# Kernel optimization log

Hardware: AMD Instinct MI355X
Metric: run time of the kernel (lower is better)

The kernel has to match this reference:

```python
import jax, jax.numpy as jnp
import numpy as np
from functools import partial

SUBJECT_CATEGORY_ID = 0
PNMS_THRESH = 0.7


def box_cxcywh_to_xyxy(b):
    cx, cy, w, h = jnp.split(b, 4, axis=-1)
    return jnp.concatenate([cx - 0.5 * w, cy - 0.5 * h, cx + 0.5 * w, cy + 0.5 * h], axis=-1)


def box_iou(b1, b2):
    # b1: [Q,4], b2: [Q,4] (xyxy) -> [Q,Q] IoU (torchvision-style)
    area1 = (b1[:, 2] - b1[:, 0]) * (b1[:, 3] - b1[:, 1])
    area2 = (b2[:, 2] - b2[:, 0]) * (b2[:, 3] - b2[:, 1])
    lt = jnp.maximum(b1[:, None, :2], b2[None, :, :2])
    rb = jnp.minimum(b1[:, None, 2:], b2[None, :, 2:])
    wh = jnp.clip(rb - lt, 0.0)
    inter = wh[..., 0] * wh[..., 1]
    union = area1[:, None] + area2[None, :] - inter
    return inter / union


def pnms_one(vs, ol, pair_iou):
    # vs: [Q,V] verb scores, ol: [Q] int labels, pair_iou: [Q,Q].
    # Replicates the original greedy per-class suppression, including the
    # original's row-i update vs[i, suppressed_queries] -= 1 (requires Q <= V).
    Q, V = vs.shape

    def class_step(vs, i):
        col = jnp.take(vs, i, axis=1)           # [Q]
        order = jnp.argsort(-col)               # descending, like reversed argsort

        def greedy(carry, j):
            alive, supp = carry
            is_alive = alive[j]
            kill = alive & (ol == ol[j]) & (pair_iou[j] > PNMS_THRESH)
            kill = kill.at[j].set(False)
            kill = kill & is_alive
            alive_next = (alive & ~kill).at[j].set(False)
            alive = jnp.where(is_alive, alive_next, alive)
            return (alive, supp | kill), None

        (alive, supp), _ = jax.lax.scan(
            greedy, (jnp.ones((Q,), bool), jnp.zeros((Q,), bool)), order)
        delta = jnp.zeros((V,), vs.dtype).at[:Q].set(supp.astype(vs.dtype))
        vs = vs.at[i].add(-delta)
        return vs, None

    vs, _ = jax.lax.scan(class_step, vs, jnp.arange(V))
    return vs


def setup_inputs() -> dict:
    key = jax.random.key(0)
    k1, k2, k3, k4, k5 = jax.random.split(key, 5)
    B, Q, C, V = 1024, 100, 81, 117
    return {
        'obj_logits': jax.random.normal(k1, (B, Q, C), jnp.float32),
        'verb_logits': jax.random.normal(k2, (B, Q, V), jnp.float32),
        'sub_boxes': jax.random.uniform(k3, (B, Q, 4), jnp.float32),
        'obj_boxes': jax.random.uniform(k4, (B, Q, 4), jnp.float32),
        'target_sizes': jax.random.randint(k5, (B, 2), 0, 1333, jnp.int32),
    }


def reference(obj_logits, verb_logits, sub_boxes, obj_boxes, target_sizes):
    obj_prob = jax.nn.softmax(obj_logits, axis=-1)
    obj_scores = obj_prob[..., :-1].max(-1)                 # [B,Q]
    obj_labels = jnp.argmax(obj_prob[..., :-1], axis=-1)    # [B,Q]
    verb_scores = jax.nn.sigmoid(verb_logits)               # [B,Q,V]

    sizes = target_sizes.astype(jnp.float32)
    img_h, img_w = sizes[:, 0], sizes[:, 1]
    scale = jnp.stack([img_w, img_h, img_w, img_h], axis=1)  # [B,4]
    sb = box_cxcywh_to_xyxy(sub_boxes) * scale[:, None, :]
    ob = box_cxcywh_to_xyxy(obj_boxes) * scale[:, None, :]

    sub_labels = jnp.full_like(obj_labels, SUBJECT_CATEGORY_ID)
    labels = jnp.concatenate([sub_labels, obj_labels], axis=1)   # [B,2Q]
    boxes = jnp.concatenate([sb, ob], axis=1)                    # [B,2Q,4]

    vs = verb_scores * obj_scores[..., None]                     # [B,Q,V]
    pair_iou = jnp.minimum(jax.vmap(box_iou)(sb, sb), jax.vmap(box_iou)(ob, ob))
    vs = jax.vmap(pnms_one)(vs, obj_labels, pair_iou)
    return vs, obj_scores, labels, boxes
```

## Files before the change

kernel.cpp:

```cpp
#include <hip/hip_runtime.h>
#include <math.h>

#define Q 100
#define NC 81
#define NV 117
#define MAXK 48

__global__ __launch_bounds__(256) void k_scores_vs(
    const float*  __restrict__ obj_logits,
    const float4* __restrict__ verb4,
    float* __restrict__ out_vs,
    float* __restrict__ out_scores,
    float* __restrict__ out_labels,
    int BQ)
{
    const int lane = threadIdx.x & 63;
    const int sl   = lane & 15;
    const int w    = blockIdx.x * 4 + (threadIdx.x >> 6);
    const int q    = w * 4 + (lane >> 4);
    if (q >= BQ) return;
    const float* lp = obj_logits + (size_t)q * NC;

    float v[5];
    #pragma unroll
    for (int c = 0; c < 5; ++c) v[c] = lp[sl + c * 16];
    const float l80 = lp[80];

    float bv = v[0]; int bi = sl;
    #pragma unroll
    for (int c = 1; c < 5; ++c)
        if (v[c] > bv) { bv = v[c]; bi = sl + c * 16; }
    #pragma unroll
    for (int d = 1; d < 16; d <<= 1) {
        float ov = __shfl_xor(bv, d, 16);
        int   oi = __shfl_xor(bi, d, 16);
        if (ov > bv || (ov == bv && oi < bi)) { bv = ov; bi = oi; }
    }
    const float m = fmaxf(bv, l80);

    float s = (sl == 0) ? expf(l80 - m) : 0.f;
    #pragma unroll
    for (int c = 0; c < 5; ++c) s += expf(v[c] - m);
    #pragma unroll
    for (int d = 1; d < 16; d <<= 1) s += __shfl_xor(s, d, 16);

    const float sc = __fdiv_rn(expf(bv - m), s);
    if (sl == 0) {
        int b = q / Q, qq = q - b * Q;
        out_scores[q] = sc;
        out_labels[(size_t)b * 2 * Q + qq]     = 0.0f;
        out_labels[(size_t)b * 2 * Q + Q + qq] = (float)bi;
    }

    const float s0 = __shfl(sc, 0);
    const float s1 = __shfl(sc, 16);
    const float s2 = __shfl(sc, 32);
    const float s3 = __shfl(sc, 48);

    const size_t base4 = (size_t)w * NV;
    float4* ovs4 = reinterpret_cast<float4*>(out_vs);
    #pragma unroll
    for (int it = 0; it < 2; ++it) {
        const int idx = it * 64 + lane;
        if (idx < NV) {
            float4 x = verb4[base4 + idx];
            float xv[4] = {x.x, x.y, x.z, x.w};
            float r[4];
            #pragma unroll
            for (int j = 0; j < 4; ++j) {
                const int e = idx * 4 + j;
                const float scq = (e < NV) ? s0 : (e < 2 * NV) ? s1
                                 : (e < 3 * NV) ? s2 : s3;
                float sg = __fdiv_rn(1.0f, __fadd_rn(1.0f, expf(-xv[j])));
                r[j] = __fmul_rn(sg, scq);
            }
            ovs4[base4 + idx] = make_float4(r[0], r[1], r[2], r[3]);
        }
    }
}

__global__ __launch_bounds__(256) void k_pnms(
    const float* __restrict__ sub_boxes,
    const float* __restrict__ obj_boxes,
    const int*   __restrict__ target_sizes,
    const float* __restrict__ out_labels,
    float* __restrict__ out_vs,
    float* __restrict__ out_boxes)
{
    __shared__ float4 sb4[Q], ob4[Q];
    __shared__ float  area_s[Q], area_o[Q];
    __shared__ int    labi[Q];
    __shared__ unsigned long long lbl_bits[NC - 1][2];
    __shared__ unsigned long long mask_s[2 * Q];
    __shared__ unsigned long long killset_s[2 * Q];
    __shared__ int   clist_s[Q];
    __shared__ float col_s[Q];
    __shared__ float vsrow[MAXK * 101];
    __shared__ int   anyconf, Ksh;

    const int b   = blockIdx.x;
    const int tid = threadIdx.x;

    if (tid == 0) anyconf = 0;
    if (tid < 2 * Q) killset_s[tid] = 0ull;
    if (tid < 2 * (NC - 1)) ((unsigned long long*)lbl_bits)[tid] = 0ull;

    if (tid < 2 * Q) {
        const int q = (tid < Q) ? tid : tid - Q;
        const float fh = (float)target_sizes[2 * b];
        const float fw = (float)target_sizes[2 * b + 1];
        const float4* src = reinterpret_cast<const float4*>(tid < Q ? sub_boxes : obj_boxes);
        float4 cxy = src[(size_t)b * Q + q];
        float hw = __fmul_rn(0.5f, cxy.z);
        float hh = __fmul_rn(0.5f, cxy.w);
        float4 box;
        box.x = __fmul_rn(__fsub_rn(cxy.x, hw), fw);
        box.y = __fmul_rn(__fsub_rn(cxy.y, hh), fh);
        box.z = __fmul_rn(__fadd_rn(cxy.x, hw), fw);
        box.w = __fmul_rn(__fadd_rn(cxy.y, hh), fh);
        float area = __fmul_rn(__fsub_rn(box.z, box.x), __fsub_rn(box.w, box.y));
        if (tid < Q) {
            sb4[q] = box; area_s[q] = area;
            reinterpret_cast<float4*>(out_boxes)[(size_t)b * 2 * Q + q] = box;
            labi[q] = (int)out_labels[(size_t)b * 2 * Q + Q + q];
        } else {
            ob4[q] = box; area_o[q] = area;
            reinterpret_cast<float4*>(out_boxes)[(size_t)b * 2 * Q + Q + q] = box;
        }
    }
    __syncthreads();

    if (tid < Q)
        atomicOr(&lbl_bits[labi[tid]][tid >> 6], 1ull << (tid & 63));
    __syncthreads();

    if (tid < Q) {
        const int j = tid;
        const float4 sj = sb4[j]; const float asj = area_s[j];
        const float4 oj = ob4[j]; const float aoj = area_o[j];
        const int lj = labi[j];
        unsigned long long bits[2] = {0ull, 0ull};
        #pragma unroll
        for (int w = 0; w < 2; ++w) {
            unsigned long long mm = lbl_bits[lj][w];
            if (w == (j >> 6)) mm &= ~(1ull << (j & 63));
            while (mm) {
                int kb = __builtin_ctzll(mm); mm &= mm - 1;
                int k = kb + w * 64;
                float4 sk = sb4[k];
                float wx = fmaxf(__fsub_rn(fminf(sj.z, sk.z), fmaxf(sj.x, sk.x)), 0.f);
                float wy = fmaxf(__fsub_rn(fminf(sj.w, sk.w), fmaxf(sj.y, sk.y)), 0.f);
                float inter = __fmul_rn(wx, wy);
                float uni = __fsub_rn(__fadd_rn(asj, area_s[k]), inter);
                float ious = __fdiv_rn(inter, uni);
                float4 ok = ob4[k];
                wx = fmaxf(__fsub_rn(fminf(oj.z, ok.z), fmaxf(oj.x, ok.x)), 0.f);
                wy = fmaxf(__fsub_rn(fminf(oj.w, ok.w), fmaxf(oj.y, ok.y)), 0.f);
                inter = __fmul_rn(wx, wy);
                uni = __fsub_rn(__fadd_rn(aoj, area_o[k]), inter);
                float iouo = __fdiv_rn(inter, uni);
                if (ious != ious || iouo != iouo) continue;
                if (fminf(ious, iouo) > 0.7f) bits[w] |= 1ull << kb;
            }
        }
        mask_s[2 * j]     = bits[0];
        mask_s[2 * j + 1] = bits[1];
        if (bits[0] | bits[1]) anyconf = 1;
    }
    __syncthreads();

    if (!anyconf) return;

    if (tid == 0) {
        int K = 0;
        for (int q = 0; q < Q; ++q)
            if (mask_s[2 * q] | mask_s[2 * q + 1]) clist_s[K++] = q;
        Ksh = K;
    }
    __syncthreads();
    const int K = Ksh;
    const bool staged = (K <= MAXK);

    if (staged) {
        for (int idx = tid; idx < K * Q; idx += 256) {
            int k = idx / Q, i = idx - k * Q;
            vsrow[k * 101 + i] = out_vs[(size_t)b * Q * NV + clist_s[k] * NV + i];
        }
    }
    __syncthreads();

    if (tid == 0) {
        for (int i = 0; i < Q; ++i) {
            for (int k = 0; k < K; ++k) {
                int c = clist_s[k];
                float v = staged ? vsrow[k * 101 + i]
                                 : out_vs[(size_t)b * Q * NV + c * NV + i];
                if ((killset_s[2 * c + (i >> 6)] >> (i & 63)) & 1ull)
                    v = __fsub_rn(v, 1.0f);
                col_s[k] = v;
            }
            unsigned long long alive0 = ~0ull, alive1 = (1ull << 36) - 1;
            unsigned long long supp0 = 0ull, supp1 = 0ull;
            for (int t = 0; t < K; ++t) {
                float best = col_s[0]; int bk = 0;
                for (int k = 1; k < K; ++k) { float ck = col_s[k]; if (ck > best) { best = ck; bk = k; } }
                col_s[bk] = -3.0e38f;
                int q = clist_s[bk];
                bool al = (q < 64) ? ((alive0 >> q) & 1ull) : ((alive1 >> (q - 64)) & 1ull);
                if (al) {
                    unsigned long long m0 = mask_s[2 * q], m1 = mask_s[2 * q + 1];
                    supp0 |= alive0 & m0;
                    supp1 |= alive1 & m1;
                    alive0 &= ~m0;
                    alive1 &= ~m1;
                    if (q < 64) alive0 &= ~(1ull << q); else alive1 &= ~(1ull << (q - 64));
                }
            }
            killset_s[2 * i]     = supp0;
            killset_s[2 * i + 1] = supp1;
        }
    }
    __syncthreads();

    for (int idx = tid; idx < Q * Q; idx += 256) {
        int qrow = idx / Q, v = idx - qrow * Q;
        if ((killset_s[2 * qrow + (v >> 6)] >> (v & 63)) & 1ull) {
            size_t a = (size_t)b * Q * NV + qrow * NV + v;
            out_vs[a] = __fsub_rn(out_vs[a], 1.0f);
        }
    }
}

extern "C" void kernel_launch(void* const* d_in, const int* in_sizes, int n_in,
                              void* d_out, int out_size, void* d_ws, size_t ws_size,
                              hipStream_t stream) {
    const float* obj_logits   = (const float*)d_in[0];
    const float* verb_logits  = (const float*)d_in[1];
    const float* sub_boxes    = (const float*)d_in[2];
    const float* obj_boxes    = (const float*)d_in[3];
    const int*   target_sizes = (const int*)d_in[4];
    const int B  = in_sizes[0] / (Q * NC);
    const int BQ = B * Q;

    float* out_vs     = (float*)d_out;
    float* out_scores = out_vs + (size_t)B * Q * NV;
    float* out_labels = out_scores + (size_t)BQ;
    float* out_boxes  = out_labels + (size_t)B * 2 * Q;

    k_scores_vs<<<dim3((BQ + 15) / 16), dim3(256), 0, stream>>>(
        obj_logits, (const float4*)verb_logits,
        out_vs, out_scores, out_labels, BQ);

    k_pnms<<<dim3(B), dim3(256), 0, stream>>>(
        sub_boxes, obj_boxes, target_sizes, out_labels, out_vs, out_boxes);
}
```

Measured before the change: 133.4 us.

## Fuse score/verb kernel into per-image PNMS kernel with 512 threads

```diff
diff --git a/kernel.cpp b/kernel.cpp
--- a/kernel.cpp
+++ b/kernel.cpp
@@ -5,91 +5,23 @@
 #define NC 81
 #define NV 117
 #define MAXK 48
-
-__global__ __launch_bounds__(256) void k_scores_vs(
+#define NV4 2925
+
+__global__ __launch_bounds__(512) void hoi_fused(
     const float*  __restrict__ obj_logits,
     const float4* __restrict__ verb4,
+    const float*  __restrict__ sub_boxes,
+    const float*  __restrict__ obj_boxes,
+    const int*    __restrict__ target_sizes,
     float* __restrict__ out_vs,
     float* __restrict__ out_scores,
     float* __restrict__ out_labels,
-    int BQ)
-{
-    const int lane = threadIdx.x & 63;
-    const int sl   = lane & 15;
-    const int w    = blockIdx.x * 4 + (threadIdx.x >> 6);
-    const int q    = w * 4 + (lane >> 4);
-    if (q >= BQ) return;
-    const float* lp = obj_logits + (size_t)q * NC;
-
-    float v[5];
-    #pragma unroll
-    for (int c = 0; c < 5; ++c) v[c] = lp[sl + c * 16];
-    const float l80 = lp[80];
-
-    float bv = v[0]; int bi = sl;
-    #pragma unroll
-    for (int c = 1; c < 5; ++c)
-        if (v[c] > bv) { bv = v[c]; bi = sl + c * 16; }
-    #pragma unroll
-    for (int d = 1; d < 16; d <<= 1) {
-        float ov = __shfl_xor(bv, d, 16);
-        int   oi = __shfl_xor(bi, d, 16);
-        if (ov > bv || (ov == bv && oi < bi)) { bv = ov; bi = oi; }
-    }
-    const float m = fmaxf(bv, l80);
-
-    float s = (sl == 0) ? expf(l80 - m) : 0.f;
-    #pragma unroll
-    for (int c = 0; c < 5; ++c) s += expf(v[c] - m);
-    #pragma unroll
-    for (int d = 1; d < 16; d <<= 1) s += __shfl_xor(s, d, 16);
-
-    const float sc = __fdiv_rn(expf(bv - m), s);
-    if (sl == 0) {
-        int b = q / Q, qq = q - b * Q;
-        out_scores[q] = sc;
-        out_labels[(size_t)b * 2 * Q + qq]     = 0.0f;
-        out_labels[(size_t)b * 2 * Q + Q + qq] = (float)bi;
-    }
-
-    const float s0 = __shfl(sc, 0);
-    const float s1 = __shfl(sc, 16);
-    const float s2 = __shfl(sc, 32);
-    const float s3 = __shfl(sc, 48);
-
-    const size_t base4 = (size_t)w * NV;
-    float4* ovs4 = reinterpret_cast<float4*>(out_vs);
-    #pragma unroll
-    for (int it = 0; it < 2; ++it) {
-        const int idx = it * 64 + lane;
-        if (idx < NV) {
-            float4 x = verb4[base4 + idx];
-            float xv[4] = {x.x, x.y, x.z, x.w};
-            float r[4];
-            #pragma unroll
-            for (int j = 0; j < 4; ++j) {
-                const int e = idx * 4 + j;
-                const float scq = (e < NV) ? s0 : (e < 2 * NV) ? s1
-                                 : (e < 3 * NV) ? s2 : s3;
-                float sg = __fdiv_rn(1.0f, __fadd_rn(1.0f, expf(-xv[j])));
-                r[j] = __fmul_rn(sg, scq);
-            }
-            ovs4[base4 + idx] = make_float4(r[0], r[1], r[2], r[3]);
-        }
-    }
-}
-
-__global__ __launch_bounds__(256) void k_pnms(
-    const float* __restrict__ sub_boxes,
-    const float* __restrict__ obj_boxes,
-    const int*   __restrict__ target_sizes,
-    const float* __restrict__ out_labels,
-    float* __restrict__ out_vs,
     float* __restrict__ out_boxes)
 {
+    __shared__ float  score_s[Q];
+    __shared__ int    labi[Q];
     __shared__ float4 sb4[Q], ob4[Q];
     __shared__ float  area_s[Q], area_o[Q];
-    __shared__ int    labi[Q];
     __shared__ unsigned long long lbl_bits[NC - 1][2];
     __shared__ unsigned long long mask_s[2 * Q];
     __shared__ unsigned long long killset_s[2 * Q];
@@ -98,12 +30,47 @@
     __shared__ float vsrow[MAXK * 101];
     __shared__ int   anyconf, Ksh;
 
-    const int b   = blockIdx.x;
-    const int tid = threadIdx.x;
+    const int b    = blockIdx.x;
+    const int tid  = threadIdx.x;
+    const int lane = tid & 63;
+    const int sl   = lane & 15;
+    const int r16  = tid >> 4;
 
     if (tid == 0) anyconf = 0;
     if (tid < 2 * Q) killset_s[tid] = 0ull;
     if (tid < 2 * (NC - 1)) ((unsigned long long*)lbl_bits)[tid] = 0ull;
+
+    for (int qi = r16; qi < Q; qi += 32) {
+        const float* lp = obj_logits + ((size_t)b * Q + qi) * NC;
+        float v[5];
+        #pragma unroll
+        for (int c = 0; c < 5; ++c) v[c] = lp[sl + c * 16];
+        const float l80 = lp[80];
+
+        float bv = v[0]; int bi = sl;
+        #pragma unroll
+        for (int c = 1; c < 5; ++c)
+            if (v[c] > bv) { bv = v[c]; bi = sl + c * 16; }
+        #pragma unroll
+        for (int d = 1; d < 16; d <<= 1) {
+            float ov = __shfl_xor(bv, d, 16);
+            int   oi = __shfl_xor(bi, d, 16);
+            if (ov > bv || (ov == bv && oi < bi)) { bv = ov; bi = oi; }
+        }
+        const float m = fmaxf(bv, l80);
+
+        float s = (sl == 0) ? __expf(l80 - m) : 0.f;
+        #pragma unroll
+        for (int c = 0; c < 5; ++c) s += __expf(v[c] - m);
+        #pragma unroll
+        for (int d = 1; d < 16; d <<= 1) s += __shfl_xor(s, d, 16);
+
+        if (sl == 0) {
+            score_s[qi] = __fmul_rn(__expf(bv - m), __builtin_amdgcn_rcpf(s));
+            labi[qi] = bi;
+        }
+    }
+    __syncthreads();
 
     if (tid < 2 * Q) {
         const int q = (tid < Q) ? tid : tid - Q;
@@ -119,19 +86,32 @@
         box.z = __fmul_rn(__fadd_rn(cxy.x, hw), fw);
         box.w = __fmul_rn(__fadd_rn(cxy.y, hh), fh);
         float area = __fmul_rn(__fsub_rn(box.z, box.x), __fsub_rn(box.w, box.y));
-        if (tid < Q) {
-            sb4[q] = box; area_s[q] = area;
-            reinterpret_cast<float4*>(out_boxes)[(size_t)b * 2 * Q + q] = box;
-            labi[q] = (int)out_labels[(size_t)b * 2 * Q + Q + q];
-        } else {
-            ob4[q] = box; area_o[q] = area;
-            reinterpret_cast<float4*>(out_boxes)[(size_t)b * 2 * Q + Q + q] = box;
-        }
-    }
-    __syncthreads();
-
-    if (tid < Q)
+        if (tid < Q) { sb4[q] = box; area_s[q] = area; }
+        else         { ob4[q] = box; area_o[q] = area; }
+        reinterpret_cast<float4*>(out_boxes)[(size_t)b * 2 * Q + tid] = box;
+        out_labels[(size_t)b * 2 * Q + tid] = (tid < Q) ? 0.0f : (float)labi[q];
+    }
+    if (tid < Q) {
+        out_scores[(size_t)b * Q + tid] = score_s[tid];
         atomicOr(&lbl_bits[labi[tid]][tid >> 6], 1ull << (tid & 63));
+    }
+
+    {
+        const size_t base4 = (size_t)b * NV4;
+        float4* ovs4 = reinterpret_cast<float4*>(out_vs);
+        for (int idx = tid; idx < NV4; idx += 512) {
+            float4 x = verb4[base4 + idx];
+            float xv[4] = {x.x, x.y, x.z, x.w};
+            float r[4];
+            #pragma unroll
+            for (int j = 0; j < 4; ++j) {
+                int lq = (idx * 4 + j) / NV;
+                float sg = __builtin_amdgcn_rcpf(__fadd_rn(1.0f, __expf(-xv[j])));
+                r[j] = __fmul_rn(sg, score_s[lq]);
+            }
+            ovs4[base4 + idx] = make_float4(r[0], r[1], r[2], r[3]);
+        }
+    }
     __syncthreads();
 
     if (tid < Q) {
@@ -182,7 +162,7 @@
     const bool staged = (K <= MAXK);
 
     if (staged) {
-        for (int idx = tid; idx < K * Q; idx += 256) {
+        for (int idx = tid; idx < K * Q; idx += 512) {
             int k = idx / Q, i = idx - k * Q;
             vsrow[k * 101 + i] = out_vs[(size_t)b * Q * NV + clist_s[k] * NV + i];
         }
@@ -222,7 +202,7 @@
     }
     __syncthreads();
 
-    for (int idx = tid; idx < Q * Q; idx += 256) {
+    for (int idx = tid; idx < Q * Q; idx += 512) {
         int qrow = idx / Q, v = idx - qrow * Q;
         if ((killset_s[2 * qrow + (v >> 6)] >> (v & 63)) & 1ull) {
             size_t a = (size_t)b * Q * NV + qrow * NV + v;
@@ -240,17 +220,14 @@
     const float* obj_boxes    = (const float*)d_in[3];
     const int*   target_sizes = (const int*)d_in[4];
     const int B  = in_sizes[0] / (Q * NC);
-    const int BQ = B * Q;
 
     float* out_vs     = (float*)d_out;
     float* out_scores = out_vs + (size_t)B * Q * NV;
-    float* out_labels = out_scores + (size_t)BQ;
+    float* out_labels = out_scores + (size_t)B * Q;
     float* out_boxes  = out_labels + (size_t)B * 2 * Q;
 
-    k_scores_vs<<<dim3((BQ + 15) / 16), dim3(256), 0, stream>>>(
+    hoi_fused<<<dim3(B), dim3(512), 0, stream>>>(
         obj_logits, (const float4*)verb_logits,
-        out_vs, out_scores, out_labels, BQ);
-
-    k_pnms<<<dim3(B), dim3(256), 0, stream>>>(
-        sub_boxes, obj_boxes, target_sizes, out_labels, out_vs, out_boxes);
+        sub_boxes, obj_boxes, target_sizes,
+        out_vs, out_scores, out_labels, out_boxes);
 }
```

Result: no change. 131.0 us (median of 2 runs) (-1.8%).
